# Performance work log

Hardware: AMD Instinct MI355X
Metric: run time of the kernel (lower is better)

The kernel has to match this reference:

```python
import jax, jax.numpy as jnp
import numpy as np

B, TX, ADIM = 64, 1024, 1024
UNITS, VOCAB, EDIM = 1024, 32000, 512
ATT = 10  # attention units hardcoded in Decoder


def setup_inputs() -> dict:
    key = jax.random.key(0)
    ks = jax.random.split(key, 20)
    s = 0.02
    return {
        "X": jax.random.randint(ks[0], (B, 1), 0, VOCAB),
        "a": jax.random.normal(ks[1], (B, TX, ADIM), jnp.float32),
        "h": jax.random.normal(ks[2], (B, UNITS), jnp.float32),
        "c": jax.random.normal(ks[3], (B, UNITS), jnp.float32),
        "emb": jax.random.normal(ks[4], (VOCAB, EDIM), jnp.float32) * s,
        "W1": jax.random.normal(ks[5], (ADIM + UNITS, ATT), jnp.float32) * s,
        "b1": jnp.zeros((ATT,), jnp.float32),
        "W2": jax.random.normal(ks[6], (ATT, ATT), jnp.float32) * s,
        "b2": jnp.zeros((ATT,), jnp.float32),
        "We": jax.random.normal(ks[7], (ATT, 1), jnp.float32) * s,
        "be": jnp.zeros((1,), jnp.float32),
        "Wx": jax.random.normal(ks[8], (ADIM + EDIM, 4 * UNITS), jnp.float32) * s,
        "Wh": jax.random.normal(ks[9], (UNITS, 4 * UNITS), jnp.float32) * s,
        "bl": jnp.zeros((4 * UNITS,), jnp.float32),
        "Wv": jax.random.normal(ks[10], (UNITS, VOCAB), jnp.float32) * s,
        "bv": jnp.zeros((VOCAB,), jnp.float32),
    }


def reference(X, a, h, c, emb, W1, b1, W2, b2, We, be, Wx, Wh, bl, Wv, bv):
    # embedding lookup: [B,1,E]
    x = emb[X]
    # Bahdanau attention: repeat h over Tx, concat with a
    hr = jnp.broadcast_to(h[:, None, :], (a.shape[0], a.shape[1], h.shape[-1]))
    ah = jnp.concatenate([a, hr], axis=-1)          # [B,Tx,A+U]
    e = ah @ W1 + b1                                 # [B,Tx,10]
    e = e @ W2 + b2                                  # [B,Tx,10]
    e = jax.nn.relu(e @ We + be)                     # [B,Tx,1]
    # NOTE: source softmaxes over last axis (size 1) -> all ones; kept faithful
    alpha = jax.nn.softmax(e, axis=-1)               # [B,Tx,1]
    context = jnp.sum(alpha * a, axis=1, keepdims=True)  # [B,1,A]
    # single-step LSTM on concat(context, embedding)
    xin = jnp.concatenate([context, x], axis=-1)[:, 0, :]  # [B,A+E]
    z = xin @ Wx + h @ Wh + bl                       # [B,4U]
    i, f, g, o = jnp.split(z, 4, axis=-1)            # Keras gate order i,f,c,o
    c_new = jax.nn.sigmoid(f) * c + jax.nn.sigmoid(i) * jnp.tanh(g)
    h_new = jax.nn.sigmoid(o) * jnp.tanh(c_new)
    y_pred = jax.nn.softmax(h_new @ Wv + bv, axis=-1)
    return (y_pred, context, jnp.squeeze(alpha), h_new, c_new)
```

## Files before the change

### kernel.cpp

```cpp
#include <hip/hip_runtime.h>
#include <hip/hip_bf16.h>
#include <math.h>

constexpr int NB    = 64;
constexpr int NTX   = 1024;
constexpr int NAD   = 1024;
constexpr int NU    = 1024;
constexpr int NE    = 512;
constexpr int NV    = 32000;
constexpr int KX    = NAD + NE;
constexpr int KTOT  = KX + NU;
constexpr int G4    = 4 * NU;
constexpr int NTC   = 16;

constexpr size_t OFF_AT  = 0;
constexpr size_t OFF_Z   = OFF_AT + (size_t)KTOT * NB;
constexpr size_t OFF_HT  = OFF_Z + (size_t)NB * G4;
constexpr size_t OFF_SCR = OFF_HT + (size_t)NU * NB;

constexpr size_t OUT_Y     = 0;
constexpr size_t OUT_CTX   = (size_t)NB * NV;
constexpr size_t OUT_ALPHA = OUT_CTX + (size_t)NB * NAD;
constexpr size_t OUT_H     = OUT_ALPHA + (size_t)NB * NTX;
constexpr size_t OUT_C     = OUT_H + (size_t)NB * NU;

__device__ __forceinline__ float sigf(float x) { return 1.0f / (1.0f + __expf(-x)); }

__global__ __launch_bounds__(256) void k_zinit(const float* __restrict__ bl,
                                               float* __restrict__ zacc) {
    int i = blockIdx.x * 256 + threadIdx.x;
    zacc[i] = bl[i & (G4 - 1)];
}

__global__ __launch_bounds__(256) void k_ctx(const float* __restrict__ a,
                                             float* __restrict__ part) {
    int tc = blockIdx.x, b = blockIdx.y, tid = threadIdx.x;
    float4 acc = make_float4(0.f, 0.f, 0.f, 0.f);
    int t0 = tc * (NTX / NTC);
    #pragma unroll 8
    for (int tt = 0; tt < NTX / NTC; ++tt) {
        const float4* row = (const float4*)(a + ((size_t)b * NTX + t0 + tt) * NAD);
        float4 v = row[tid];
        acc.x += v.x; acc.y += v.y; acc.z += v.z; acc.w += v.w;
    }
    float4* p4 = (float4*)(part + ((size_t)tc * NB + b) * NAD + tid * 4);
    *p4 = acc;
}

__global__ __launch_bounds__(128) void k_ctx_fin(const float* __restrict__ part,
                                                 const int* __restrict__ X,
                                                 const float* __restrict__ emb,
                                                 const float* __restrict__ h,
                                                 float* __restrict__ At,
                                                 float* __restrict__ out_ctx,
                                                 float* __restrict__ out_alpha) {
    int b = blockIdx.x, tid = threadIdx.x;
    int d0 = tid * 8;
    float s[8] = {};
    for (int tc = 0; tc < NTC; ++tc) {
        const float* p = part + ((size_t)tc * NB + b) * NAD + d0;
        #pragma unroll
        for (int i = 0; i < 8; ++i) s[i] += p[i];
    }
    #pragma unroll
    for (int i = 0; i < 8; ++i) {
        At[(size_t)(d0 + i) * NB + b] = s[i];
        out_ctx[(size_t)b * NAD + d0 + i] = s[i];
    }
    int row = X[b];
    for (int j = tid; j < NE; j += 128)
        At[(size_t)(NAD + j) * NB + b] = emb[(size_t)row * NE + j];
    for (int j = tid; j < NU; j += 128)
        At[(size_t)(KX + j) * NB + b] = h[(size_t)b * NU + j];
    for (int j = tid; j < NTX; j += 128)
        out_alpha[(size_t)b * NTX + j] = 1.0f;
}

__global__ __launch_bounds__(256) void k_zgemm(const float* __restrict__ At,
                                               const float* __restrict__ Wx,
                                               const float* __restrict__ Wh,
                                               float* __restrict__ zacc) {
    int tid = threadIdx.x;
    int u = blockIdx.x * 64 + (tid & 63);
    int b0 = __builtin_amdgcn_readfirstlane(tid >> 6) * 16;
    int k0 = blockIdx.y * (KTOT / 8);
    float acc[16] = {};
    for (int kk0 = 0; kk0 < KTOT / 8; kk0 += 8) {
        float w[8];
        #pragma unroll
        for (int j = 0; j < 8; ++j) {
            int k = k0 + kk0 + j;
            w[j] = (k < KX) ? Wx[(size_t)k * G4 + u]
                            : Wh[(size_t)(k - KX) * G4 + u];
        }
        #pragma unroll
        for (int j = 0; j < 8; ++j) {
            const float* ap = At + (size_t)(k0 + kk0 + j) * NB + b0;
            #pragma unroll
            for (int i = 0; i < 16; ++i) acc[i] = fmaf(ap[i], w[j], acc[i]);
        }
    }
    #pragma unroll
    for (int i = 0; i < 16; ++i)
        atomicAdd(&zacc[(size_t)(b0 + i) * G4 + u], acc[i]);
}

__global__ __launch_bounds__(256) void k_gates(const float* __restrict__ zacc,
                                               const float* __restrict__ c,
                                               float* __restrict__ out_h,
                                               float* __restrict__ out_c,
                                               float* __restrict__ Ht) {
    int b = blockIdx.x, tid = threadIdx.x;
    const float* z = zacc + (size_t)b * G4;
    #pragma unroll
    for (int l = 0; l < 4; ++l) {
        int j = tid * 4 + l;
        float zi = z[j], zf = z[NU + j], zg = z[2 * NU + j], zo = z[3 * NU + j];
        float cf = c[(size_t)b * NU + j];
        float cn = sigf(zf) * cf + sigf(zi) * tanhf(zg);
        float hn = sigf(zo) * tanhf(cn);
        out_c[(size_t)b * NU + j] = cn;
        out_h[(size_t)b * NU + j] = hn;
        Ht[(size_t)j * NB + b] = hn;
    }
}

__global__ __launch_bounds__(256) void k_vgemm(const float* __restrict__ Ht,
                                               const float* __restrict__ Wv,
                                               const float* __restrict__ bv,
                                               float* __restrict__ logits) {
    int tid = threadIdx.x;
    int u = blockIdx.x * 64 + (tid & 63);
    int b0 = __builtin_amdgcn_readfirstlane(tid >> 6) * 16;
    float acc[16] = {};
    const float* wcol = Wv + u;
    for (int k0 = 0; k0 < NU; k0 += 8) {
        float w[8];
        #pragma unroll
        for (int j = 0; j < 8; ++j)
            w[j] = wcol[(size_t)(k0 + j) * NV];
        #pragma unroll
        for (int j = 0; j < 8; ++j) {
            const float* ap = Ht + (size_t)(k0 + j) * NB + b0;
            #pragma unroll
            for (int i = 0; i < 16; ++i) acc[i] = fmaf(ap[i], w[j], acc[i]);
        }
    }
    float bvu = bv[u];
    #pragma unroll
    for (int i = 0; i < 16; ++i)
        logits[(size_t)(b0 + i) * NV + u] = acc[i] + bvu;
}

__global__ __launch_bounds__(256) void k_softmax(const float* __restrict__ logits,
                                                 float* __restrict__ y) {
    __shared__ float red[256];
    int b = blockIdx.x, tid = threadIdx.x;
    const float* row = logits + (size_t)b * NV;
    float m = -1e30f;
    for (int i = tid; i < NV; i += 256) m = fmaxf(m, row[i]);
    red[tid] = m; __syncthreads();
    for (int s = 128; s > 0; s >>= 1) {
        if (tid < s) red[tid] = fmaxf(red[tid], red[tid + s]);
        __syncthreads();
    }
    float M = red[0]; __syncthreads();
    float ssum = 0.0f;
    for (int i = tid; i < NV; i += 256) ssum += __expf(row[i] - M);
    red[tid] = ssum; __syncthreads();
    for (int s = 128; s > 0; s >>= 1) {
        if (tid < s) red[tid] += red[tid + s];
        __syncthreads();
    }
    float inv = 1.0f / red[0];
    for (int i = tid; i < NV; i += 256)
        y[(size_t)b * NV + i] = __expf(row[i] - M) * inv;
}

extern "C" void kernel_launch(void* const* d_in, const int* in_sizes, int n_in,
                              void* d_out, int out_size, void* d_ws, size_t ws_size,
                              hipStream_t stream) {
    const int*   X   = (const int*)d_in[0];
    const float* a   = (const float*)d_in[1];
    const float* h   = (const float*)d_in[2];
    const float* c   = (const float*)d_in[3];
    const float* emb = (const float*)d_in[4];
    const float* Wx  = (const float*)d_in[11];
    const float* Wh  = (const float*)d_in[12];
    const float* bl  = (const float*)d_in[13];
    const float* Wv  = (const float*)d_in[14];
    const float* bv  = (const float*)d_in[15];

    float* out = (float*)d_out;
    float* ws  = (float*)d_ws;
    float* At      = ws + OFF_AT;
    float* zacc    = ws + OFF_Z;
    float* Ht      = ws + OFF_HT;
    float* scratch = ws + OFF_SCR;

    float* out_y     = out + OUT_Y;
    float* out_ctx   = out + OUT_CTX;
    float* out_alpha = out + OUT_ALPHA;
    float* out_h     = out + OUT_H;
    float* out_c     = out + OUT_C;

    hipLaunchKernelGGL(k_zinit,   dim3(1024),     dim3(256), 0, stream, bl, zacc);
    hipLaunchKernelGGL(k_ctx,     dim3(NTC, NB),  dim3(256), 0, stream, a, scratch);
    hipLaunchKernelGGL(k_ctx_fin, dim3(NB),       dim3(128), 0, stream, scratch, X, emb, h, At, out_ctx, out_alpha);
    hipLaunchKernelGGL(k_zgemm,   dim3(G4/64, 8), dim3(256), 0, stream, At, Wx, Wh, zacc);
    hipLaunchKernelGGL(k_gates,   dim3(NB),       dim3(256), 0, stream, zacc, c, out_h, out_c, Ht);
    hipLaunchKernelGGL(k_vgemm,   dim3(NV/64),    dim3(256), 0, stream, Ht, Wv, bv, scratch);
    hipLaunchKernelGGL(k_softmax, dim3(NB),       dim3(256), 0, stream, scratch, out_y);
}
```

Before: 696.2 us.

## Widen GEMM column tiles, double-buffer weight loads, split-K vgemm, split softmax

Both weight GEMMs now give each lane two output columns through float2 loads and double-buffer the weight rows in registers, so loads overlap the FMAs. The z GEMM uses 16 K-splits instead of 8. The vocab GEMM uses 512-thread blocks that split K in two and reduce through shared memory. The single-block-per-row softmax becomes two kernels that spread each row over 4 blocks using an online max/sum merge. This adds an extra launch and more atomics in exchange for more parallelism and better memory efficiency.

```diff
diff --git a/kernel.cpp b/kernel.cpp
--- a/kernel.cpp
+++ b/kernel.cpp
@@ -12,11 +12,13 @@
 constexpr int KTOT  = KX + NU;
 constexpr int G4    = 4 * NU;
 constexpr int NTC   = 16;
+constexpr int ZKS   = 16;
 
 constexpr size_t OFF_AT  = 0;
 constexpr size_t OFF_Z   = OFF_AT + (size_t)KTOT * NB;
 constexpr size_t OFF_HT  = OFF_Z + (size_t)NB * G4;
 constexpr size_t OFF_SCR = OFF_HT + (size_t)NU * NB;
+constexpr size_t OFF_SM  = OFF_SCR + (size_t)NB * NV;
 
 constexpr size_t OUT_Y     = 0;
 constexpr size_t OUT_CTX   = (size_t)NB * NV;
@@ -76,33 +78,55 @@
         out_alpha[(size_t)b * NTX + j] = 1.0f;
 }
 
+#define ZG_LD(buf, g)                                                          \
+    _Pragma("unroll")                                                          \
+    for (int j = 0; j < 8; ++j) {                                              \
+        int k = kbeg + (g) * 8 + j;                                            \
+        const float2* base = (k < KX) ? (Wx2 + (size_t)k * (G4 / 2))           \
+                                      : (Wh2 + (size_t)(k - KX) * (G4 / 2));   \
+        buf[j] = base[uq];                                                     \
+    }
+
+#define ZG_FMA(buf, g)                                                         \
+    _Pragma("unroll")                                                          \
+    for (int j = 0; j < 8; ++j) {                                              \
+        const float* ap = At + (size_t)(kbeg + (g) * 8 + j) * NB + b0;         \
+        _Pragma("unroll")                                                      \
+        for (int i = 0; i < 16; ++i) {                                         \
+            acc[i].x = fmaf(ap[i], buf[j].x, acc[i].x);                        \
+            acc[i].y = fmaf(ap[i], buf[j].y, acc[i].y);                        \
+        }                                                                      \
+    }
+
 __global__ __launch_bounds__(256) void k_zgemm(const float* __restrict__ At,
                                                const float* __restrict__ Wx,
                                                const float* __restrict__ Wh,
                                                float* __restrict__ zacc) {
     int tid = threadIdx.x;
-    int u = blockIdx.x * 64 + (tid & 63);
+    int lane = tid & 63;
     int b0 = __builtin_amdgcn_readfirstlane(tid >> 6) * 16;
-    int k0 = blockIdx.y * (KTOT / 8);
-    float acc[16] = {};
-    for (int kk0 = 0; kk0 < KTOT / 8; kk0 += 8) {
-        float w[8];
-        #pragma unroll
-        for (int j = 0; j < 8; ++j) {
-            int k = k0 + kk0 + j;
-            w[j] = (k < KX) ? Wx[(size_t)k * G4 + u]
-                            : Wh[(size_t)(k - KX) * G4 + u];
-        }
-        #pragma unroll
-        for (int j = 0; j < 8; ++j) {
-            const float* ap = At + (size_t)(k0 + kk0 + j) * NB + b0;
-            #pragma unroll
-            for (int i = 0; i < 16; ++i) acc[i] = fmaf(ap[i], w[j], acc[i]);
-        }
-    }
-    #pragma unroll
-    for (int i = 0; i < 16; ++i)
-        atomicAdd(&zacc[(size_t)(b0 + i) * G4 + u], acc[i]);
+    int uq = blockIdx.x * 64 + lane;
+    int kbeg = blockIdx.y * (KTOT / ZKS);
+    const float2* Wx2 = (const float2*)Wx;
+    const float2* Wh2 = (const float2*)Wh;
+    float2 acc[16];
+    #pragma unroll
+    for (int i = 0; i < 16; ++i) acc[i] = make_float2(0.f, 0.f);
+    float2 bA[8], bB[8];
+    constexpr int NG = (KTOT / ZKS) / 8;
+    ZG_LD(bA, 0);
+    for (int g = 0; g < NG; g += 2) {
+        ZG_LD(bB, g + 1);
+        ZG_FMA(bA, g);
+        if (g + 2 < NG) ZG_LD(bA, g + 2);
+        ZG_FMA(bB, g + 1);
+    }
+    int u0 = uq * 2;
+    #pragma unroll
+    for (int i = 0; i < 16; ++i) {
+        atomicAdd(&zacc[(size_t)(b0 + i) * G4 + u0],     acc[i].x);
+        atomicAdd(&zacc[(size_t)(b0 + i) * G4 + u0 + 1], acc[i].y);
+    }
 }
 
 __global__ __launch_bounds__(256) void k_gates(const float* __restrict__ zacc,
@@ -125,56 +149,142 @@
     }
 }
 
-__global__ __launch_bounds__(256) void k_vgemm(const float* __restrict__ Ht,
+#define VG_LD(buf, g)                                                          \
+    _Pragma("unroll")                                                          \
+    for (int j = 0; j < 8; ++j)                                                \
+        buf[j] = wp[(size_t)((g) * 8 + j) * (NV / 2)];
+
+#define VG_FMA(buf, g)                                                         \
+    _Pragma("unroll")                                                          \
+    for (int j = 0; j < 8; ++j) {                                              \
+        const float* ap = Ht + (size_t)(kbeg + (g) * 8 + j) * NB + b0;         \
+        _Pragma("unroll")                                                      \
+        for (int i = 0; i < 16; ++i) {                                         \
+            acc[i].x = fmaf(ap[i], buf[j].x, acc[i].x);                        \
+            acc[i].y = fmaf(ap[i], buf[j].y, acc[i].y);                        \
+        }                                                                      \
+    }
+
+__global__ __launch_bounds__(512) void k_vgemm(const float* __restrict__ Ht,
                                                const float* __restrict__ Wv,
                                                const float* __restrict__ bv,
                                                float* __restrict__ logits) {
+    __shared__ float red[4][64][33];
     int tid = threadIdx.x;
-    int u = blockIdx.x * 64 + (tid & 63);
-    int b0 = __builtin_amdgcn_readfirstlane(tid >> 6) * 16;
-    float acc[16] = {};
-    const float* wcol = Wv + u;
-    for (int k0 = 0; k0 < NU; k0 += 8) {
-        float w[8];
+    int lane = tid & 63;
+    int w  = __builtin_amdgcn_readfirstlane(tid >> 6);
+    int bw = w & 3;
+    int kc = w >> 2;
+    int b0 = bw * 16;
+    int uq = blockIdx.x * 64 + lane;
+    int kbeg = kc * (NU / 2);
+    const float2* Wv2 = (const float2*)Wv;
+    const float2* wp = Wv2 + (size_t)kbeg * (NV / 2) + uq;
+    float2 acc[16];
+    #pragma unroll
+    for (int i = 0; i < 16; ++i) acc[i] = make_float2(0.f, 0.f);
+    float2 bA[8], bB[8];
+    constexpr int NG = (NU / 2) / 8;
+    VG_LD(bA, 0);
+    for (int g = 0; g < NG; g += 2) {
+        VG_LD(bB, g + 1);
+        VG_FMA(bA, g);
+        if (g + 2 < NG) VG_LD(bA, g + 2);
+        VG_FMA(bB, g + 1);
+    }
+    if (kc == 1) {
         #pragma unroll
-        for (int j = 0; j < 8; ++j)
-            w[j] = wcol[(size_t)(k0 + j) * NV];
+        for (int i = 0; i < 16; ++i) {
+            red[bw][lane][2 * i]     = acc[i].x;
+            red[bw][lane][2 * i + 1] = acc[i].y;
+        }
+    }
+    __syncthreads();
+    if (kc == 0) {
+        float2 bvv = ((const float2*)bv)[uq];
         #pragma unroll
-        for (int j = 0; j < 8; ++j) {
-            const float* ap = Ht + (size_t)(k0 + j) * NB + b0;
-            #pragma unroll
-            for (int i = 0; i < 16; ++i) acc[i] = fmaf(ap[i], w[j], acc[i]);
+        for (int i = 0; i < 16; ++i) {
+            float2 r;
+            r.x = acc[i].x + red[bw][lane][2 * i]     + bvv.x;
+            r.y = acc[i].y + red[bw][lane][2 * i + 1] + bvv.y;
+            ((float2*)(logits + (size_t)(b0 + i) * NV))[uq] = r;
         }
     }
-    float bvu = bv[u];
-    #pragma unroll
-    for (int i = 0; i < 16; ++i)
-        logits[(size_t)(b0 + i) * NV + u] = acc[i] + bvu;
-}
-
-__global__ __launch_bounds__(256) void k_softmax(const float* __restrict__ logits,
-                                                 float* __restrict__ y) {
-    __shared__ float red[256];
-    int b = blockIdx.x, tid = threadIdx.x;
-    const float* row = logits + (size_t)b * NV;
+}
+
+__global__ __launch_bounds__(256) void k_smax1(const float* __restrict__ logits,
+                                               float* __restrict__ smp) {
+    __shared__ float lm[4], ls[4];
+    int q = blockIdx.x, b = blockIdx.y, tid = threadIdx.x;
+    const float4* row4 = (const float4*)(logits + (size_t)b * NV) + q * 2000;
+    float4 v[8];
+    #pragma unroll
+    for (int j = 0; j < 8; ++j) {
+        int idx = tid + 256 * j;
+        v[j] = (idx < 2000) ? row4[idx]
+                            : make_float4(-1e30f, -1e30f, -1e30f, -1e30f);
+    }
     float m = -1e30f;
-    for (int i = tid; i < NV; i += 256) m = fmaxf(m, row[i]);
-    red[tid] = m; __syncthreads();
-    for (int s = 128; s > 0; s >>= 1) {
-        if (tid < s) red[tid] = fmaxf(red[tid], red[tid + s]);
-        __syncthreads();
-    }
-    float M = red[0]; __syncthreads();
-    float ssum = 0.0f;
-    for (int i = tid; i < NV; i += 256) ssum += __expf(row[i] - M);
-    red[tid] = ssum; __syncthreads();
-    for (int s = 128; s > 0; s >>= 1) {
-        if (tid < s) red[tid] += red[tid + s];
-        __syncthreads();
-    }
-    float inv = 1.0f / red[0];
-    for (int i = tid; i < NV; i += 256)
-        y[(size_t)b * NV + i] = __expf(row[i] - M) * inv;
+    #pragma unroll
+    for (int j = 0; j < 8; ++j)
+        m = fmaxf(m, fmaxf(fmaxf(v[j].x, v[j].y), fmaxf(v[j].z, v[j].w)));
+    float s = 0.0f;
+    #pragma unroll
+    for (int j = 0; j < 8; ++j)
+        s += __expf(v[j].x - m) + __expf(v[j].y - m) +
+             __expf(v[j].z - m) + __expf(v[j].w - m);
+    #pragma unroll
+    for (int off = 32; off > 0; off >>= 1) {
+        float om = __shfl_xor(m, off);
+        float os = __shfl_xor(s, off);
+        float M = fmaxf(m, om);
+        s = s * __expf(m - M) + os * __expf(om - M);
+        m = M;
+    }
+    int wv = tid >> 6, lane = tid & 63;
+    if (lane == 0) { lm[wv] = m; ls[wv] = s; }
+    __syncthreads();
+    if (tid == 0) {
+        float M = fmaxf(fmaxf(lm[0], lm[1]), fmaxf(lm[2], lm[3]));
+        float S = ls[0] * __expf(lm[0] - M) + ls[1] * __expf(lm[1] - M) +
+                  ls[2] * __expf(lm[2] - M) + ls[3] * __expf(lm[3] - M);
+        smp[b * 4 + q]       = M;
+        smp[256 + b * 4 + q] = S;
+    }
+}
+
+__global__ __launch_bounds__(256) void k_smax2(const float* __restrict__ logits,
+                                               const float* __restrict__ smp,
+                                               float* __restrict__ y) {
+    int q = blockIdx.x, b = blockIdx.y, tid = threadIdx.x;
+    float m0 = smp[b * 4], m1 = smp[b * 4 + 1],
+          m2 = smp[b * 4 + 2], m3 = smp[b * 4 + 3];
+    float M = fmaxf(fmaxf(m0, m1), fmaxf(m2, m3));
+    float S = smp[256 + b * 4]     * __expf(m0 - M) +
+              smp[256 + b * 4 + 1] * __expf(m1 - M) +
+              smp[256 + b * 4 + 2] * __expf(m2 - M) +
+              smp[256 + b * 4 + 3] * __expf(m3 - M);
+    float inv = 1.0f / S;
+    const float4* row4 = (const float4*)(logits + (size_t)b * NV) + q * 2000;
+    float4* y4 = (float4*)(y + (size_t)b * NV) + q * 2000;
+    float4 v[8];
+    #pragma unroll
+    for (int j = 0; j < 8; ++j) {
+        int idx = tid + 256 * j;
+        v[j] = (idx < 2000) ? row4[idx] : make_float4(0.f, 0.f, 0.f, 0.f);
+    }
+    #pragma unroll
+    for (int j = 0; j < 8; ++j) {
+        int idx = tid + 256 * j;
+        if (idx < 2000) {
+            float4 o;
+            o.x = __expf(v[j].x - M) * inv;
+            o.y = __expf(v[j].y - M) * inv;
+            o.z = __expf(v[j].z - M) * inv;
+            o.w = __expf(v[j].w - M) * inv;
+            y4[idx] = o;
+        }
+    }
 }
 
 extern "C" void kernel_launch(void* const* d_in, const int* in_sizes, int n_in,
@@ -197,6 +307,7 @@
     float* zacc    = ws + OFF_Z;
     float* Ht      = ws + OFF_HT;
     float* scratch = ws + OFF_SCR;
+    float* smp     = ws + OFF_SM;
 
     float* out_y     = out + OUT_Y;
     float* out_ctx   = out + OUT_CTX;
@@ -204,11 +315,12 @@
     float* out_h     = out + OUT_H;
     float* out_c     = out + OUT_C;
 
-    hipLaunchKernelGGL(k_zinit,   dim3(1024),     dim3(256), 0, stream, bl, zacc);
-    hipLaunchKernelGGL(k_ctx,     dim3(NTC, NB),  dim3(256), 0, stream, a, scratch);
-    hipLaunchKernelGGL(k_ctx_fin, dim3(NB),       dim3(128), 0, stream, scratch, X, emb, h, At, out_ctx, out_alpha);
-    hipLaunchKernelGGL(k_zgemm,   dim3(G4/64, 8), dim3(256), 0, stream, At, Wx, Wh, zacc);
-    hipLaunchKernelGGL(k_gates,   dim3(NB),       dim3(256), 0, stream, zacc, c, out_h, out_c, Ht);
-    hipLaunchKernelGGL(k_vgemm,   dim3(NV/64),    dim3(256), 0, stream, Ht, Wv, bv, scratch);
-    hipLaunchKernelGGL(k_softmax, dim3(NB),       dim3(256), 0, stream, scratch, out_y);
-}
+    hipLaunchKernelGGL(k_zinit,   dim3(1024),        dim3(256), 0, stream, bl, zacc);
+    hipLaunchKernelGGL(k_ctx,     dim3(NTC, NB),     dim3(256), 0, stream, a, scratch);
+    hipLaunchKernelGGL(k_ctx_fin, dim3(NB),          dim3(128), 0, stream, scratch, X, emb, h, At, out_ctx, out_alpha);
+    hipLaunchKernelGGL(k_zgemm,   dim3(G4/128, ZKS), dim3(256), 0, stream, At, Wx, Wh, zacc);
+    hipLaunchKernelGGL(k_gates,   dim3(NB),          dim3(256), 0, stream, zacc, c, out_h, out_c, Ht);
+    hipLaunchKernelGGL(k_vgemm,   dim3(NV/128),      dim3(512), 0, stream, Ht, Wv, bv, scratch);
+    hipLaunchKernelGGL(k_smax1,   dim3(4, NB),       dim3(256), 0, stream, scratch, smp);
+    hipLaunchKernelGGL(k_smax2,   dim3(4, NB),       dim3(256), 0, stream, scratch, smp, out_y);
+}
```

New measurement: 686.3 us. No clear change (-1.4%).
